# Optimization experiments

Hardware: AMD Instinct MI355X
Metric: run time of the kernel (lower is better)

The kernel has to match this reference:

```python
import jax, jax.numpy as jnp
import numpy as np

N, IN_DIM, OUT_DIM = 8192, 128, 64
NEG_INF = -9e15

def setup_inputs() -> dict:
    key = jax.random.key(0)
    k1, k2, k3, k4 = jax.random.split(key, 4)
    h = jax.random.normal(k1, (N, IN_DIM), dtype=jnp.float32)
    adj = jax.random.randint(k2, (N, N), 0, 2, dtype=jnp.int32)
    W = jax.random.normal(k3, (IN_DIM, OUT_DIM), dtype=jnp.float32) * (1.0 / np.sqrt(IN_DIM))
    a = jax.random.normal(k4, (2 * OUT_DIM,), dtype=jnp.float32)
    return {"h": h, "adj": adj, "W": W, "a": a}

def reference(h, adj, W, a):
    Wh = h @ W  # [N, F]
    F_ = Wh.shape[1]
    # additive decomposition of cat([Wh_i, Wh_j]) @ a == Wh_i@a1 + Wh_j@a2
    e_src = Wh @ a[:F_]   # [N]
    e_dst = Wh @ a[F_:]   # [N]
    e = jax.nn.leaky_relu(e_src[:, None] + e_dst[None, :], negative_slope=0.01)  # [N, N]
    attention = jnp.where(adj > 0, e, jnp.float32(NEG_INF))
    attention = jax.nn.softmax(attention, axis=1)
    h_prime = attention @ Wh  # [N, F]
    return jax.nn.elu(h_prime)
```

## Files before the change

### kernel.cpp

```cpp
#include <hip/hip_runtime.h>
#include <hip/hip_bf16.h>

typedef __attribute__((ext_vector_type(8))) short short8;
typedef __attribute__((ext_vector_type(4))) float f32x4;

#define NROW 8192
#define FDIM 64
#define INDIM 128
#define BM 128
#define SPLITS 16
#define MBOUND 48.0f
#define L2E 1.44269504f

static __device__ __forceinline__ short bfb(float x) {
  __hip_bfloat16 b = __float2bfloat16(x);
  return *reinterpret_cast<short*>(&b);
}
static __device__ __forceinline__ float lrelu(float x) { return fmaxf(x, 0.01f * x); }

__global__ __launch_bounds__(256) void k_wh(const float* __restrict__ h,
                                            const float* __restrict__ W,
                                            const float* __restrict__ a,
                                            __hip_bfloat16* __restrict__ WhT,
                                            float* __restrict__ s,
                                            float* __restrict__ d) {
  const int i = blockIdx.x * 4 + (threadIdx.x >> 6);
  const int f = threadIdx.x & 63;
  const float* hrow = h + (size_t)i * INDIM;
  float acc = 0.f;
#pragma unroll 8
  for (int k = 0; k < INDIM; ++k) acc = fmaf(hrow[k], W[k * FDIM + f], acc);
  WhT[(size_t)f * NROW + i] = __float2bfloat16(acc);
  float p1 = acc * a[f];
  float p2 = acc * a[FDIM + f];
#pragma unroll
  for (int m = 32; m; m >>= 1) {
    p1 += __shfl_xor(p1, m, 64);
    p2 += __shfl_xor(p2, m, 64);
  }
  if (f == 0) { s[i] = p1; d[i] = p2; }
}

__global__ __launch_bounds__(256) void k_main(const int* __restrict__ adj,
                                              const __hip_bfloat16* __restrict__ WhT,
                                              const float* __restrict__ sArr,
                                              const float* __restrict__ dArr,
                                              __hip_bfloat16* __restrict__ accp,
                                              float* __restrict__ Zp) {
  const int t = threadIdx.x;
  const int w = t >> 6, l = t & 63;
  const int lr = l & 15;
  const int lk = l >> 4;
  const int panel = blockIdx.x / SPLITS;
  const int split = blockIdx.x - panel * SPLITS;
  const int row0 = panel * BM + w * 32;
  const int jspan = NROW / SPLITS;
  const int j0 = split * jspan;
  const int nchunk = jspan / 64;

  const float s0 = sArr[row0 + lr];
  const float s1 = sArr[row0 + 16 + lr];
  const float sm0 = -lrelu(s0 + MBOUND) * L2E;
  const float sm1 = -lrelu(s1 + MBOUND) * L2E;

  f32x4 acc[2][4], accZ[2];
#pragma unroll
  for (int ri = 0; ri < 2; ++ri) {
    accZ[ri] = (f32x4){0.f, 0.f, 0.f, 0.f};
#pragma unroll
    for (int nf = 0; nf < 4; ++nf) acc[ri][nf] = (f32x4){0.f, 0.f, 0.f, 0.f};
  }

  short8 bones;
#pragma unroll
  for (int q = 0; q < 8; ++q) bones[q] = (short)0x3F80;

  const int* adjp = adj + (size_t)row0 * NROW + j0 + l;
  const float* dp = dArr + j0 + lk * 8;
  const __hip_bfloat16* bbase = WhT + (size_t)lr * NROW + j0 + lk * 8;

  for (int c = 0; c < nchunk; ++c) {
    const int off = c * 64;

    unsigned long long M0 = 0ull, M1 = 0ull;
    {
      int av[16];
#pragma unroll
      for (int r = 0; r < 16; ++r)
        av[r] = __builtin_nontemporal_load(adjp + (size_t)r * NROW + off);
#pragma unroll
      for (int r = 0; r < 16; ++r) {
        unsigned long long b = __ballot(av[r] > 0);
        M0 = (lr == r) ? b : M0;
      }
#pragma unroll
      for (int r = 0; r < 16; ++r)
        av[r] = __builtin_nontemporal_load(adjp + (size_t)(16 + r) * NROW + off);
#pragma unroll
      for (int r = 0; r < 16; ++r) {
        unsigned long long b = __ballot(av[r] > 0);
        M1 = (lr == r) ? b : M1;
      }
    }

#pragma unroll
    for (int ks = 0; ks < 2; ++ks) {
      const int jo = off + ks * 32;
      const unsigned int y0 = (unsigned int)(M0 >> (ks * 32 + lk * 8)) & 0xffu;
      const unsigned int y1 = (unsigned int)(M1 >> (ks * 32 + lk * 8)) & 0xffu;

      short8 b0 = *(const short8*)(bbase + jo);
      short8 b1 = *(const short8*)(bbase + jo + 16 * NROW);
      short8 b2 = *(const short8*)(bbase + jo + 32 * NROW);
      short8 b3 = *(const short8*)(bbase + jo + 48 * NROW);

      float dj[8];
      *(float4*)&dj[0] = *(const float4*)(dp + jo);
      *(float4*)&dj[4] = *(const float4*)(dp + jo + 4);

      short8 pa0, pa1;
#pragma unroll
      for (int q = 0; q < 8; ++q) {
        const float dq = dj[q];
        float e0 = exp2f(fmaf(lrelu(s0 + dq), L2E, sm0));
        float e1 = exp2f(fmaf(lrelu(s1 + dq), L2E, sm1));
        pa0[q] = bfb(((y0 >> q) & 1u) ? e0 : 0.f);
        pa1[q] = bfb(((y1 >> q) & 1u) ? e1 : 0.f);
      }

      acc[0][0] = __builtin_amdgcn_mfma_f32_16x16x32_bf16(pa0, b0, acc[0][0], 0, 0, 0);
      acc[0][1] = __builtin_amdgcn_mfma_f32_16x16x32_bf16(pa0, b1, acc[0][1], 0, 0, 0);
      acc[0][2] = __builtin_amdgcn_mfma_f32_16x16x32_bf16(pa0, b2, acc[0][2], 0, 0, 0);
      acc[0][3] = __builtin_amdgcn_mfma_f32_16x16x32_bf16(pa0, b3, acc[0][3], 0, 0, 0);
      accZ[0]   = __builtin_amdgcn_mfma_f32_16x16x32_bf16(pa0, bones, accZ[0], 0, 0, 0);
      acc[1][0] = __builtin_amdgcn_mfma_f32_16x16x32_bf16(pa1, b0, acc[1][0], 0, 0, 0);
      acc[1][1] = __builtin_amdgcn_mfma_f32_16x16x32_bf16(pa1, b1, acc[1][1], 0, 0, 0);
      acc[1][2] = __builtin_amdgcn_mfma_f32_16x16x32_bf16(pa1, b2, acc[1][2], 0, 0, 0);
      acc[1][3] = __builtin_amdgcn_mfma_f32_16x16x32_bf16(pa1, b3, acc[1][3], 0, 0, 0);
      accZ[1]   = __builtin_amdgcn_mfma_f32_16x16x32_bf16(pa1, bones, accZ[1], 0, 0, 0);
    }
  }

  if (lr == 0) {
    float* zb = Zp + (size_t)blockIdx.x * BM + w * 32;
#pragma unroll
    for (int q = 0; q < 4; ++q) {
      zb[lk * 4 + q] = accZ[0][q];
      zb[16 + lk * 4 + q] = accZ[1][q];
    }
  }

  __hip_bfloat16* ab = accp + (size_t)blockIdx.x * (BM * 64);
#pragma unroll
  for (int ri = 0; ri < 2; ++ri)
#pragma unroll
    for (int nf = 0; nf < 4; ++nf)
#pragma unroll
      for (int q = 0; q < 4; ++q)
        ab[(w * 32 + ri * 16 + lk * 4 + q) * 64 + nf * 16 + lr] =
            __float2bfloat16(acc[ri][nf][q]);
}

__global__ __launch_bounds__(256) void k_combine(const __hip_bfloat16* __restrict__ accp,
                                                 const float* __restrict__ Zp,
                                                 float* __restrict__ out) {
  const int idx = blockIdx.x * 256 + threadIdx.x;
  const int r = idx >> 6, f = idx & 63;
  const int panel = r >> 7, rl = r & 127;
  float sum = 0.f, z = 0.f;
#pragma unroll
  for (int sp = 0; sp < SPLITS; ++sp) {
    const int b = panel * SPLITS + sp;
    sum += __bfloat162float(accp[(size_t)b * (BM * 64) + rl * 64 + f]);
    z += Zp[(size_t)b * BM + rl];
  }
  const float v = sum / z;
  out[idx] = (v > 0.f) ? v : expm1f(v);
}

extern "C" void kernel_launch(void* const* d_in, const int* in_sizes, int n_in,
                              void* d_out, int out_size, void* d_ws, size_t ws_size,
                              hipStream_t stream) {
  const float* h = (const float*)d_in[0];
  const int* adj = (const int*)d_in[1];
  const float* W = (const float*)d_in[2];
  const float* a = (const float*)d_in[3];
  float* out = (float*)d_out;

  const int npanel = NROW / BM;
  const int nblk = npanel * SPLITS;

  char* p = (char*)d_ws;
  __hip_bfloat16* WhT = (__hip_bfloat16*)p;
  float* s = (float*)(p + 1048576);
  float* d = (float*)(p + 1048576 + 32768);
  float* Zp = (float*)(p + 1048576 + 65536);
  __hip_bfloat16* accp =
      (__hip_bfloat16*)((char*)Zp + (size_t)nblk * BM * 4);

  hipLaunchKernelGGL(k_wh, dim3(NROW / 4), dim3(256), 0, stream, h, W, a, WhT, s, d);
  hipLaunchKernelGGL(k_main, dim3(nblk), dim3(256), 0, stream, adj, WhT, s, d, accp, Zp);
  hipLaunchKernelGGL(k_combine, dim3(out_size / 256), dim3(256), 0, stream, accp, Zp, out);
}
```

Baseline: 116.8 us.

## Replace ones-MFMA row-sum with scalar accumulation and use inline-asm nontemporal adj loads

Drops the two extra MFMAs per k-step that computed the softmax denominator against a ones vector. Each lane now sums its fp32 masked weights in registers, and a cross-lane shuffle reduction runs at the end. The denominator now uses unrounded fp32 weights while the numerator still uses bf16-rounded ones, which adds a small numeric mismatch. The adj loads are rewritten as inline-asm global_load_dword with sc1 nt cache hints plus explicit waitcnt and sched barriers, and launch bounds now request 4 waves per SIMD, which may constrain register allocation.

```diff
diff --git a/kernel.cpp b/kernel.cpp
--- a/kernel.cpp
+++ b/kernel.cpp
@@ -9,6 +9,7 @@
 #define INDIM 128
 #define BM 128
 #define SPLITS 16
+#define NPANEL (NROW / BM)
 #define MBOUND 48.0f
 #define L2E 1.44269504f
 
@@ -41,12 +42,12 @@
   if (f == 0) { s[i] = p1; d[i] = p2; }
 }
 
-__global__ __launch_bounds__(256) void k_main(const int* __restrict__ adj,
-                                              const __hip_bfloat16* __restrict__ WhT,
-                                              const float* __restrict__ sArr,
-                                              const float* __restrict__ dArr,
-                                              __hip_bfloat16* __restrict__ accp,
-                                              float* __restrict__ Zp) {
+__global__ __launch_bounds__(256, 4) void k_main(const int* __restrict__ adj,
+                                                 const __hip_bfloat16* __restrict__ WhT,
+                                                 const float* __restrict__ sArr,
+                                                 const float* __restrict__ dArr,
+                                                 __hip_bfloat16* __restrict__ accp,
+                                                 float* __restrict__ Zp) {
   const int t = threadIdx.x;
   const int w = t >> 6, l = t & 63;
   const int lr = l & 15;
@@ -63,17 +64,12 @@
   const float sm0 = -lrelu(s0 + MBOUND) * L2E;
   const float sm1 = -lrelu(s1 + MBOUND) * L2E;
 
-  f32x4 acc[2][4], accZ[2];
-#pragma unroll
-  for (int ri = 0; ri < 2; ++ri) {
-    accZ[ri] = (f32x4){0.f, 0.f, 0.f, 0.f};
+  f32x4 acc[2][4];
+#pragma unroll
+  for (int ri = 0; ri < 2; ++ri)
 #pragma unroll
     for (int nf = 0; nf < 4; ++nf) acc[ri][nf] = (f32x4){0.f, 0.f, 0.f, 0.f};
-  }
-
-  short8 bones;
-#pragma unroll
-  for (int q = 0; q < 8; ++q) bones[q] = (short)0x3F80;
+  float z0 = 0.f, z1 = 0.f;
 
   const int* adjp = adj + (size_t)row0 * NROW + j0 + l;
   const float* dp = dArr + j0 + lk * 8;
@@ -86,16 +82,24 @@
     {
       int av[16];
 #pragma unroll
-      for (int r = 0; r < 16; ++r)
-        av[r] = __builtin_nontemporal_load(adjp + (size_t)r * NROW + off);
+      for (int r = 0; r < 16; ++r) {
+        unsigned long long addr = (unsigned long long)(adjp + (size_t)r * NROW + off);
+        asm volatile("global_load_dword %0, %1, off sc1 nt" : "=v"(av[r]) : "v"(addr));
+      }
+      asm volatile("s_waitcnt vmcnt(0)" ::: "memory");
+      __builtin_amdgcn_sched_barrier(0);
 #pragma unroll
       for (int r = 0; r < 16; ++r) {
         unsigned long long b = __ballot(av[r] > 0);
         M0 = (lr == r) ? b : M0;
       }
 #pragma unroll
-      for (int r = 0; r < 16; ++r)
-        av[r] = __builtin_nontemporal_load(adjp + (size_t)(16 + r) * NROW + off);
+      for (int r = 0; r < 16; ++r) {
+        unsigned long long addr = (unsigned long long)(adjp + (size_t)(16 + r) * NROW + off);
+        asm volatile("global_load_dword %0, %1, off sc1 nt" : "=v"(av[r]) : "v"(addr));
+      }
+      asm volatile("s_waitcnt vmcnt(0)" ::: "memory");
+      __builtin_amdgcn_sched_barrier(0);
 #pragma unroll
       for (int r = 0; r < 16; ++r) {
         unsigned long long b = __ballot(av[r] > 0);
@@ -124,30 +128,32 @@
         const float dq = dj[q];
         float e0 = exp2f(fmaf(lrelu(s0 + dq), L2E, sm0));
         float e1 = exp2f(fmaf(lrelu(s1 + dq), L2E, sm1));
-        pa0[q] = bfb(((y0 >> q) & 1u) ? e0 : 0.f);
-        pa1[q] = bfb(((y1 >> q) & 1u) ? e1 : 0.f);
+        float w0 = ((y0 >> q) & 1u) ? e0 : 0.f;
+        float w1 = ((y1 >> q) & 1u) ? e1 : 0.f;
+        z0 += w0;
+        z1 += w1;
+        pa0[q] = bfb(w0);
+        pa1[q] = bfb(w1);
       }
 
       acc[0][0] = __builtin_amdgcn_mfma_f32_16x16x32_bf16(pa0, b0, acc[0][0], 0, 0, 0);
       acc[0][1] = __builtin_amdgcn_mfma_f32_16x16x32_bf16(pa0, b1, acc[0][1], 0, 0, 0);
       acc[0][2] = __builtin_amdgcn_mfma_f32_16x16x32_bf16(pa0, b2, acc[0][2], 0, 0, 0);
       acc[0][3] = __builtin_amdgcn_mfma_f32_16x16x32_bf16(pa0, b3, acc[0][3], 0, 0, 0);
-      accZ[0]   = __builtin_amdgcn_mfma_f32_16x16x32_bf16(pa0, bones, accZ[0], 0, 0, 0);
       acc[1][0] = __builtin_amdgcn_mfma_f32_16x16x32_bf16(pa1, b0, acc[1][0], 0, 0, 0);
       acc[1][1] = __builtin_amdgcn_mfma_f32_16x16x32_bf16(pa1, b1, acc[1][1], 0, 0, 0);
       acc[1][2] = __builtin_amdgcn_mfma_f32_16x16x32_bf16(pa1, b2, acc[1][2], 0, 0, 0);
       acc[1][3] = __builtin_amdgcn_mfma_f32_16x16x32_bf16(pa1, b3, acc[1][3], 0, 0, 0);
-      accZ[1]   = __builtin_amdgcn_mfma_f32_16x16x32_bf16(pa1, bones, accZ[1], 0, 0, 0);
     }
   }
 
-  if (lr == 0) {
-    float* zb = Zp + (size_t)blockIdx.x * BM + w * 32;
-#pragma unroll
-    for (int q = 0; q < 4; ++q) {
-      zb[lk * 4 + q] = accZ[0][q];
-      zb[16 + lk * 4 + q] = accZ[1][q];
-    }
+  z0 += __shfl_xor(z0, 16, 64);
+  z0 += __shfl_xor(z0, 32, 64);
+  z1 += __shfl_xor(z1, 16, 64);
+  z1 += __shfl_xor(z1, 32, 64);
+  if (l < 16) {
+    Zp[(size_t)blockIdx.x * BM + w * 32 + lr] = z0;
+    Zp[(size_t)blockIdx.x * BM + w * 32 + 16 + lr] = z1;
   }
 
   __hip_bfloat16* ab = accp + (size_t)blockIdx.x * (BM * 64);
@@ -187,8 +193,7 @@
   const float* a = (const float*)d_in[3];
   float* out = (float*)d_out;
 
-  const int npanel = NROW / BM;
-  const int nblk = npanel * SPLITS;
+  const int nblk = NPANEL * SPLITS;
 
   char* p = (char*)d_ws;
   __hip_bfloat16* WhT = (__hip_bfloat16*)p;
```

After: 213.8 us. 83.0% more time.
